# Optimization experiments

Hardware: AMD Instinct MI355X
Metric: run time of the kernel (lower is better)

The kernel has to match this reference:

```python
import jax, jax.numpy as jnp
import numpy as np

N, C, CI, H, W = 4, 512, 256, 64, 64  # batch, in_channels, inter_channels, spatial
EPS = 1e-5


def conv1x1(x, w, b):
    # x: (N,C,H,W), w: (O,C), b: (O,)
    return jnp.einsum('nchw,oc->nohw', x, w) + b[None, :, None, None]


def setup_inputs() -> dict:
    key = jax.random.key(0)
    ks = jax.random.split(key, 11)
    s = 0.02
    return {
        'x': jax.random.normal(ks[0], (N, C, H, W), dtype=jnp.float32),
        'g_w': jax.random.normal(ks[1], (CI, C), dtype=jnp.float32) * s,
        'g_b': jax.random.normal(ks[2], (CI,), dtype=jnp.float32) * s,
        'theta_w': jax.random.normal(ks[3], (CI, C), dtype=jnp.float32) * s,
        'theta_b': jax.random.normal(ks[4], (CI,), dtype=jnp.float32) * s,
        'phi_w': jax.random.normal(ks[5], (CI, C), dtype=jnp.float32) * s,
        'phi_b': jax.random.normal(ks[6], (CI,), dtype=jnp.float32) * s,
        'wz_w': jax.random.normal(ks[7], (C, CI), dtype=jnp.float32) * s,
        'wz_b': jax.random.normal(ks[8], (C,), dtype=jnp.float32) * s,
        'bn_gamma': jax.random.normal(ks[9], (C,), dtype=jnp.float32) * 0.1 + 1.0,
        'bn_beta': jax.random.normal(ks[10], (C,), dtype=jnp.float32) * 0.1,
    }


def reference(x, g_w, g_b, theta_w, theta_b, phi_w, phi_b, wz_w, wz_b, bn_gamma, bn_beta):
    # NLBlockND.forward_self, mode='embedded', dimension=2, bn_layer=True
    n = x.shape[0]
    L = x.shape[2] * x.shape[3]  # H*W tokens
    g_x = conv1x1(x, g_w, g_b).reshape(n, CI, L)          # (N,Ci,L)
    theta_x = conv1x1(x, theta_w, theta_b).reshape(n, CI, L)
    phi_x = conv1x1(x, phi_w, phi_b).reshape(n, CI, L)
    f = jnp.einsum('ncl,ncm->nlm', theta_x, phi_x)        # (N,L,L) = theta^T @ phi
    f_div_C = jax.nn.softmax(f, axis=-1)
    y = jnp.einsum('nlm,ncm->ncl', f_div_C, g_x)          # (N,Ci,L) = (attn @ g)^T
    y = y.reshape(n, CI, x.shape[2], x.shape[3])
    w_y = conv1x1(y, wz_w, wz_b)                          # (N,C,H,W)
    # BatchNorm2d, training-mode batch statistics (biased variance)
    mean = jnp.mean(w_y, axis=(0, 2, 3), keepdims=True)
    var = jnp.var(w_y, axis=(0, 2, 3), keepdims=True)
    w_y = (w_y - mean) * jax.lax.rsqrt(var + EPS)
    w_y = w_y * bn_gamma[None, :, None, None] + bn_beta[None, :, None, None]
    return w_y + x
```

## Files before the change

### kernel.cpp

```cpp
#include <hip/hip_runtime.h>
#include <hip/hip_bf16.h>
#include <hip/hip_fp16.h>


#define NB    4
#define CDIM  512
#define CIDIM 256
#define LDIM  4096
#define BN_EPS 1e-5f
#define LOG2E 1.4426950408889634f

typedef unsigned short u16;
typedef __attribute__((ext_vector_type(8))) short short8;
typedef __attribute__((ext_vector_type(4))) float f32x4;
typedef __attribute__((ext_vector_type(16))) float f32x16;

#define WY_OFF    0
#define THPH_OFF  8388608
#define G_OFF     12582912
#define Y_OFF     14680064
#define WTS_OFF   16777216
#define BIAS2_OFF 17039360
#define ML_OFF    17039872
#define ST_OFF    17105408

__device__ __forceinline__ u16 f2b(float f) {
    union { float f; unsigned u; } v; v.f = f;
    return (u16)((v.u + 0x7FFFu + ((v.u >> 16) & 1u)) >> 16);
}

__device__ __forceinline__ float b2f(u16 x) {
    return __uint_as_float((unsigned)x << 16);
}

__device__ __forceinline__ unsigned pack2(float a, float b) {
    return (unsigned)f2b(a) | ((unsigned)f2b(b) << 16);
}

__device__ __forceinline__ float fast_exp2(float x) {
#if __has_builtin(__builtin_amdgcn_exp2f)
    return __builtin_amdgcn_exp2f(x);
#else
    float r; asm("v_exp_f32 %0, %1" : "=v"(r) : "v"(x)); return r;
#endif
}

__device__ __forceinline__ void gl_lds16(const u16* g, u16* l) {
    __builtin_amdgcn_global_load_lds(
        (const __attribute__((address_space(1))) void*)g,
        (__attribute__((address_space(3))) void*)l, 16, 0, 0);
}

__global__ void transpose_x(const float* __restrict__ x, u16* __restrict__ xt) {
    __shared__ float tile[32][33];
    int n = blockIdx.z;
    int l0 = blockIdx.x * 32, c0 = blockIdx.y * 32;
    const float* xn = x + (size_t)n * CDIM * LDIM;
    u16* xtn = xt + (size_t)n * LDIM * CDIM;
    int tx = threadIdx.x, ty = threadIdx.y;
#pragma unroll
    for (int k = 0; k < 4; k++)
        tile[ty + 8 * k][tx] = xn[(size_t)(c0 + ty + 8 * k) * LDIM + l0 + tx];
    __syncthreads();
#pragma unroll
    for (int k = 0; k < 4; k++)
        xtn[(size_t)(l0 + ty + 8 * k) * CDIM + c0 + tx] = f2b(tile[tx][ty + 8 * k]);
}

__global__ void cast_w(const float* __restrict__ gw, const float* __restrict__ tw,
                       const float* __restrict__ pw, const float* __restrict__ zw,
                       u16* __restrict__ out,
                       const float* __restrict__ tb, const float* __restrict__ pb,
                       float* __restrict__ bc) {
    int idx = blockIdx.x * 256 + threadIdx.x;
    if (idx < 4 * 131072) {
        int seg = idx >> 17, off = idx & 131071;
        const float* s = (seg == 0) ? gw : (seg == 1) ? tw : (seg == 2) ? pw : zw;
        float v = s[off];
        if (seg == 1) v *= LOG2E;
        out[idx] = f2b(v);
    } else {
        int i = idx - 4 * 131072;
        if (i < 256) bc[i] = tb[i] * LOG2E;
        else if (i < 512) bc[i] = pb[i - 256];
    }
}

template <int BIAS_MODE, bool OUT_BF16>
__global__ __launch_bounds__(256)
void gemm_nt(const u16* __restrict__ A, const u16* __restrict__ B,
             void* __restrict__ Dv, const float* __restrict__ bias,
             int K, int lda, int ldb, int ldd,
             long batchA, long batchB, long batchD) {
    __shared__ __align__(16) u16 As[2][128 * 32];
    __shared__ __align__(16) u16 Bs[2][128 * 32];
    int z = blockIdx.z;
    A += (size_t)z * batchA;
    B += (size_t)z * batchB;

    int tid = threadIdx.x, lane = tid & 63, wave = tid >> 6;
    int n0 = blockIdx.x * 128, m0 = blockIdx.y * 128;
    int wr = wave >> 1, wc = wave & 1;

    f32x4 acc[4][4];
#pragma unroll
    for (int i = 0; i < 4; i++)
#pragma unroll
        for (int j = 0; j < 4; j++) acc[i][j] = (f32x4){0.f, 0.f, 0.f, 0.f};

    int sr = wave * 16 + (lane >> 2);
    int ss = ((lane & 3) ^ ((lane >> 2) & 3)) * 8;
    const u16* Ag0 = A + (size_t)(m0 + sr) * lda + ss;
    const u16* Ag1 = A + (size_t)(m0 + 64 + sr) * lda + ss;
    const u16* Bg0 = B + (size_t)(n0 + sr) * ldb + ss;
    const u16* Bg1 = B + (size_t)(n0 + 64 + sr) * ldb + ss;
    int sdst = wave * 16 * 32;

    int koff = ((lane >> 4) ^ (lane & 3)) * 8;
    int ra = (wr * 64 + (lane & 15)) * 32 + koff;
    int rb = (wc * 64 + (lane & 15)) * 32 + koff;

#define GSTAGE(bi, k0_) do {                                                   \
    gl_lds16(Ag0 + (k0_), &As[bi][sdst]);                                      \
    gl_lds16(Ag1 + (k0_), &As[bi][sdst + 2048]);                               \
    gl_lds16(Bg0 + (k0_), &Bs[bi][sdst]);                                      \
    gl_lds16(Bg1 + (k0_), &Bs[bi][sdst + 2048]);                               \
} while (0)

    GSTAGE(0, 0);
    int cur = 0;

    for (int k0 = 0; k0 < K; k0 += 32) {
        __syncthreads();
        if (k0 + 32 < K) GSTAGE(cur ^ 1, k0 + 32);

        short8 af[4], bf[4];
#pragma unroll
        for (int mt = 0; mt < 4; mt++) af[mt] = *(const short8*)&As[cur][ra + mt * 512];
#pragma unroll
        for (int nt = 0; nt < 4; nt++) bf[nt] = *(const short8*)&Bs[cur][rb + nt * 512];
#pragma unroll
        for (int mt = 0; mt < 4; mt++)
#pragma unroll
            for (int nt = 0; nt < 4; nt++)
                acc[mt][nt] = __builtin_amdgcn_mfma_f32_16x16x32_bf16(
                    af[mt], bf[nt], acc[mt][nt], 0, 0, 0);
        cur ^= 1;
    }
#undef GSTAGE

#pragma unroll
    for (int mt = 0; mt < 4; mt++) {
        int mg = m0 + wr * 64 + mt * 16 + (lane >> 4) * 4;
#pragma unroll
        for (int nt = 0; nt < 4; nt++) {
            int ng = n0 + wc * 64 + nt * 16 + (lane & 15);
#pragma unroll
            for (int r = 0; r < 4; r++) {
                float v = acc[mt][nt][r];
                if (BIAS_MODE == 1) v += bias[mg + r];
                if (BIAS_MODE == 2) v += bias[ng];
                if (OUT_BF16) {
                    u16* D = (u16*)Dv + (size_t)z * batchD;
                    D[(size_t)(mg + r) * ldd + ng] = f2b(v);
                } else {
                    float* D = (float*)Dv + (size_t)z * batchD;
                    D[(size_t)(mg + r) * ldd + ng] = v;
                }
            }
        }
    }
}

__global__ __launch_bounds__(256, 2)
void flash_attn(const u16* __restrict__ THPH, const u16* __restrict__ G,
                u16* __restrict__ OPB, unsigned* __restrict__ ML4) {
    __shared__ __align__(16) u16 Ks[2][32 * 256];
    __shared__ __align__(16) u16 Vs[2][256 * 32];

    int b = blockIdx.x;
    int n = b & 3;
    int jh = (b >> 2) & 3;
    int qt = b >> 4;
    int q0 = qt * 128;

    const u16* TH = THPH + (size_t)n * LDIM * 512;
    const u16* PH = TH + 256;
    const u16* Gn = G + (size_t)n * LDIM * CIDIM;
    u16* OPh = OPB + ((size_t)jh * NB + n) * CIDIM * LDIM;
    unsigned* MLh = ML4 + ((size_t)jh * NB + n) * LDIM;

    int tid = threadIdx.x, lane = tid & 63, w = tid >> 6;
    int h = lane >> 5, lq = lane & 31, l7 = lane & 7;

    short8 qf[16];
    {
        const u16* qb = TH + (size_t)(q0 + w * 32 + lq) * 512 + h * 8;
#pragma unroll
        for (int c = 0; c < 16; c++) qf[c] = *(const short8*)(qb + c * 16);
    }

    f32x16 o[8];
#pragma unroll
    for (int i = 0; i < 8; i++)
#pragma unroll
        for (int e = 0; e < 16; e++) o[i][e] = 0.f;
    float m = -3e38f, lsum = 0.f;

    int krh = lane >> 5;
    int ksl = lane & 31;
    int vr = lane >> 2;
    int vsl = (lane & 3) ^ ((lane >> 3) & 3);

#define STAGE(bufi, jt_) do {                                                  \
    int j0_ = jh * 1024 + (jt_) * 32;                                          \
    _Pragma("unroll")                                                          \
    for (int i = 0; i < 4; i++) {                                              \
        int r = w * 8 + 2 * i + krh;                                           \
        int s = ksl ^ (r & 7);                                                 \
        gl_lds16(PH + (size_t)(j0_ + r) * 512 + s * 8,                         \
                 &Ks[bufi][(w * 8 + 2 * i) * 256]);                            \
    }                                                                          \
    _Pragma("unroll")                                                          \
    for (int i = 0; i < 4; i++) {                                              \
        int r = w * 64 + 16 * i + vr;                                          \
        gl_lds16(Gn + (size_t)r * LDIM + j0_ + vsl * 8,                        \
                 &Vs[bufi][(w * 64 + 16 * i) * 32]);                           \
    }                                                                          \
} while (0)

    STAGE(0, 0);
    int cur = 0;

#pragma unroll 1
    for (int jt = 0; jt < 32; jt++) {
        __syncthreads();
        if (jt + 1 < 32) STAGE(cur ^ 1, jt + 1);

        const u16* kb = Ks[cur];
        const u16* vb = Vs[cur];

        f32x16 svx, svy;
#pragma unroll
        for (int e = 0; e < 16; e++) { svx[e] = 0.f; svy[e] = 0.f; }
#pragma unroll
        for (int c = 0; c < 8; c++) {
            int slot = (c * 2 + h) ^ l7;
            short8 ka = *(const short8*)&kb[lq * 256 + slot * 8];
            svx = __builtin_amdgcn_mfma_f32_32x32x16_bf16(ka, qf[c], svx, 0, 0, 0);
        }
#pragma unroll
        for (int c = 8; c < 16; c++) {
            int slot = (c * 2 + h) ^ l7;
            short8 ka = *(const short8*)&kb[lq * 256 + slot * 8];
            svy = __builtin_amdgcn_mfma_f32_32x32x16_bf16(ka, qf[c], svy, 0, 0, 0);
        }
        f32x16 sv = svx + svy;

        float tm = sv[0];
#pragma unroll
        for (int r = 1; r < 16; r++) tm = fmaxf(tm, sv[r]);
        tm = fmaxf(tm, __shfl_xor(tm, 32, 64));

        if (!__all(tm <= m + 11.5f)) {
            float mnew = fmaxf(m, tm);
            float al = fast_exp2(m - mnew);
            m = mnew;
            lsum *= al;
#pragma unroll
            for (int i = 0; i < 8; i++)
#pragma unroll
                for (int e = 0; e < 16; e++) o[i][e] *= al;
        }

        float rs = 0.f;
#pragma unroll
        for (int r = 0; r < 16; r++) {
            float p = fast_exp2(sv[r] - m);
            sv[r] = p;
            rs += p;
        }
        lsum += rs + __shfl_xor(rs, 32, 64);

#pragma unroll
        for (int st = 0; st < 2; st++) {
            int r0 = 8 * st;
            float e0 = sv[r0 + 0], e1 = sv[r0 + 1];
            float e2 = sv[r0 + 2], e3 = sv[r0 + 3];
            float e4 = sv[r0 + 4], e5 = sv[r0 + 5];
            float e6 = sv[r0 + 6], e7 = sv[r0 + 7];
            unsigned own_a = h ? pack2(e4, e5) : pack2(e0, e1);
            unsigned own_b = h ? pack2(e6, e7) : pack2(e2, e3);
            unsigned snd_a = h ? pack2(e0, e1) : pack2(e4, e5);
            unsigned snd_b = h ? pack2(e2, e3) : pack2(e6, e7);
            unsigned rcv_a = __shfl_xor(snd_a, 32, 64);
            unsigned rcv_b = __shfl_xor(snd_b, 32, 64);
            union { unsigned u[4]; short8 v; } pf;
            pf.u[0] = h ? rcv_a : own_a;
            pf.u[1] = h ? rcv_b : own_b;
            pf.u[2] = h ? own_a : rcv_a;
            pf.u[3] = h ? own_b : rcv_b;
            int slot = (st * 2 + h) ^ ((lq >> 1) & 3);
            short8 va[8];
#pragma unroll
            for (int cit = 0; cit < 8; cit++)
                va[cit] = *(const short8*)&vb[(cit * 32 + lq) * 32 + slot * 8];
#pragma unroll
            for (int cit = 0; cit < 8; cit++)
                o[cit] = __builtin_amdgcn_mfma_f32_32x32x16_bf16(va[cit], pf.v, o[cit], 0, 0, 0);
        }
        cur ^= 1;
    }

    int q = q0 + w * 32 + lq;
    if (h == 0) {
        unsigned pm = (unsigned)__half_as_ushort(__float2half(m));
        unsigned pl = (unsigned)__half_as_ushort(__float2half(lsum));
        MLh[q] = pm | (pl << 16);
    }
#pragma unroll
    for (int cit = 0; cit < 8; cit++)
#pragma unroll
        for (int rr = 0; rr < 16; rr++) {
            int ci = cit * 32 + (rr & 3) + 8 * (rr >> 2) + 4 * h;
            OPh[(size_t)ci * LDIM + q] = f2b(o[cit][rr]);
        }
#undef STAGE
}

__global__ void merge_y(const u16* __restrict__ OPB, const unsigned* __restrict__ ML4,
                        u16* __restrict__ Y) {
    __shared__ u16 tile[32][33];
    int nn = blockIdx.z;
    int l0 = blockIdx.x * 32, ci0 = blockIdx.y * 32;
    int tx = threadIdx.x, ty = threadIdx.y;
    int l = l0 + tx;

    float mq[4], lq[4];
#pragma unroll
    for (int q = 0; q < 4; q++) {
        unsigned u = ML4[((size_t)q * NB + nn) * LDIM + l];
        mq[q] = __half2float(__ushort_as_half((unsigned short)(u & 0xffff)));
        lq[q] = __half2float(__ushort_as_half((unsigned short)(u >> 16)));
    }
    float M = fmaxf(fmaxf(mq[0], mq[1]), fmaxf(mq[2], mq[3]));
    float wq[4];
    float den = 0.f;
#pragma unroll
    for (int q = 0; q < 4; q++) {
        wq[q] = fast_exp2(mq[q] - M);
        den += lq[q] * wq[q];
    }
    float inv = 1.f / den;
#pragma unroll
    for (int q = 0; q < 4; q++) wq[q] *= inv;

#pragma unroll
    for (int k = 0; k < 4; k++) {
        int ci = ci0 + ty + 8 * k;
        float acc = 0.f;
#pragma unroll
        for (int q = 0; q < 4; q++)
            acc += b2f(OPB[((size_t)q * NB + nn) * CIDIM * LDIM + (size_t)ci * LDIM + l]) * wq[q];
        tile[ty + 8 * k][tx] = f2b(acc);
    }
    __syncthreads();
    u16* Yn = Y + (size_t)nn * LDIM * CIDIM;
#pragma unroll
    for (int k = 0; k < 4; k++)
        Yn[(size_t)(l0 + ty + 8 * k) * CIDIM + ci0 + tx] = tile[tx][ty + 8 * k];
}

__global__ void bn_stats_kernel(const float* __restrict__ WY, float* __restrict__ stats) {
    int o = blockIdx.x, tid = threadIdx.x, lane = tid & 63, wave = tid >> 6;
    float s = 0.f, s2 = 0.f;
    for (int n = 0; n < NB; n++) {
        const float4* p = (const float4*)(WY + (size_t)(n * CDIM + o) * LDIM);
        for (int i = tid; i < LDIM / 4; i += 256) {
            float4 v = p[i];
            s += v.x + v.y + v.z + v.w;
            s2 += v.x * v.x + v.y * v.y + v.z * v.z + v.w * v.w;
        }
    }
    for (int o2 = 32; o2 > 0; o2 >>= 1) {
        s += __shfl_xor(s, o2, 64);
        s2 += __shfl_xor(s2, o2, 64);
    }
    __shared__ float rs[4], rs2[4];
    if (lane == 0) { rs[wave] = s; rs2[wave] = s2; }
    __syncthreads();
    if (tid == 0) {
        float S = rs[0] + rs[1] + rs[2] + rs[3];
        float S2 = rs2[0] + rs2[1] + rs2[2] + rs2[3];
        const float cnt = (float)(NB * LDIM);
        float mean = S / cnt;
        float var = S2 / cnt - mean * mean;
        stats[o] = mean;
        stats[CDIM + o] = rsqrtf(var + BN_EPS);
    }
}

__global__ void bn_apply_kernel(const float* __restrict__ WY, const float* __restrict__ stats,
                                const float* __restrict__ x,
                                const float* __restrict__ gamma, const float* __restrict__ beta,
                                float* __restrict__ out) {
    int i4 = blockIdx.x * 256 + threadIdx.x;
    int o = (i4 >> 10) & (CDIM - 1);
    float m = stats[o], is = stats[CDIM + o];
    float ga = gamma[o], be = beta[o];
    float4 w = ((const float4*)WY)[i4];
    float4 xv = ((const float4*)x)[i4];
    float4 r;
    r.x = (w.x - m) * is * ga + be + xv.x;
    r.y = (w.y - m) * is * ga + be + xv.y;
    r.z = (w.z - m) * is * ga + be + xv.z;
    r.w = (w.w - m) * is * ga + be + xv.w;
    ((float4*)out)[i4] = r;
}

extern "C" void kernel_launch(void* const* d_in, const int* in_sizes, int n_in,
                              void* d_out, int out_size, void* d_ws, size_t ws_size,
                              hipStream_t stream) {
    const float* x   = (const float*)d_in[0];
    const float* gw  = (const float*)d_in[1];
    const float* gb  = (const float*)d_in[2];
    const float* tw  = (const float*)d_in[3];
    const float* tb  = (const float*)d_in[4];
    const float* pw  = (const float*)d_in[5];
    const float* pb  = (const float*)d_in[6];
    const float* zw  = (const float*)d_in[7];
    const float* zb  = (const float*)d_in[8];
    const float* bng = (const float*)d_in[9];
    const float* bnb = (const float*)d_in[10];
    float* out = (float*)d_out;
    float* ws  = (float*)d_ws;

    float*    WY   = ws + WY_OFF;
    u16*      xT   = (u16*)(ws + WY_OFF);
    u16*      OPB  = (u16*)(ws + WY_OFF);
    u16*      THPH = (u16*)(ws + THPH_OFF);
    u16*      G    = (u16*)(ws + G_OFF);
    u16*      Y    = (u16*)(ws + Y_OFF);
    u16*      WB   = (u16*)(ws + WTS_OFF);
    float*    BC   = ws + BIAS2_OFF;
    unsigned* ML4  = (unsigned*)(ws + ML_OFF);
    float*    ST   = ws + ST_OFF;

    const long LC   = (long)LDIM * CDIM;
    const long LCI  = (long)LDIM * CIDIM;
    const long L512 = (long)LDIM * 512;
    const long CL   = (long)CDIM * LDIM;

    transpose_x<<<dim3(LDIM / 32, CDIM / 32, NB), dim3(32, 8), 0, stream>>>(x, xT);
    cast_w<<<2050, 256, 0, stream>>>(gw, tw, pw, zw, WB, tb, pb, BC);

    gemm_nt<2, true><<<dim3(4, 32, NB), 256, 0, stream>>>(
        xT, WB + 131072, THPH, BC, CDIM, CDIM, CDIM, 512, LC, 0, L512);
    gemm_nt<1, true><<<dim3(32, 2, NB), 256, 0, stream>>>(
        WB, xT, G, gb, CDIM, CDIM, CDIM, LDIM, 0, LC, LCI);

    flash_attn<<<dim3(512), 256, 0, stream>>>(THPH, G, OPB, ML4);
    merge_y<<<dim3(LDIM / 32, CIDIM / 32, NB), dim3(32, 8), 0, stream>>>(OPB, ML4, Y);

    gemm_nt<1, false><<<dim3(32, 4, NB), 256, 0, stream>>>(
        WB + 393216, Y, (void*)WY, zb, CIDIM, CIDIM, CIDIM, LDIM, 0, LCI, CL);

    bn_stats_kernel<<<dim3(CDIM), 256, 0, stream>>>(WY, ST);
    bn_apply_kernel<<<dim3(NB * CDIM * LDIM / 4 / 256), 256, 0, stream>>>(
        WY, ST, x, bng, bnb, out);
}
```

Baseline: 300.1 us.

## Fuse BatchNorm statistics into output GEMM epilogue and simplify attention MFMA chains

Per-channel sum and sum-of-squares are now accumulated in the epilogue of the final W_z GEMM. Each block reduces them with lane shuffles and shared-memory atomics, then adds them into global stats with atomics, and a tiny finalize kernel computes mean and rstd. This removes the separate bn_stats pass, which re-read the full 32 MB fp32 WY tensor. The flash-attention QK loop now uses a single MFMA accumulator chain instead of two, and V fragments are loaded inside the PV loop, which lowers register pressure but gives up some ILP. The global float atomics make the reduction order nondeterministic, and E[x^2]-mean^2 carries some precision risk.

Measured after the change: 275.7 us. -8.1%, faster.

```diff
diff --git a/kernel.cpp b/kernel.cpp
--- a/kernel.cpp
+++ b/kernel.cpp
@@ -71,7 +71,7 @@
                        const float* __restrict__ pw, const float* __restrict__ zw,
                        u16* __restrict__ out,
                        const float* __restrict__ tb, const float* __restrict__ pb,
-                       float* __restrict__ bc) {
+                       float* __restrict__ bc, float* __restrict__ st) {
     int idx = blockIdx.x * 256 + threadIdx.x;
     if (idx < 4 * 131072) {
         int seg = idx >> 17, off = idx & 131071;
@@ -83,17 +83,20 @@
         int i = idx - 4 * 131072;
         if (i < 256) bc[i] = tb[i] * LOG2E;
         else if (i < 512) bc[i] = pb[i - 256];
-    }
-}
-
-template <int BIAS_MODE, bool OUT_BF16>
+        else if (i < 1536) st[i - 512] = 0.f;
+    }
+}
+
+template <int BIAS_MODE, bool OUT_BF16, bool FUSE_STATS>
 __global__ __launch_bounds__(256)
 void gemm_nt(const u16* __restrict__ A, const u16* __restrict__ B,
              void* __restrict__ Dv, const float* __restrict__ bias,
+             float* __restrict__ stats,
              int K, int lda, int ldb, int ldd,
              long batchA, long batchB, long batchD) {
     __shared__ __align__(16) u16 As[2][128 * 32];
     __shared__ __align__(16) u16 Bs[2][128 * 32];
+    __shared__ float sred[256];
     int z = blockIdx.z;
     A += (size_t)z * batchA;
     B += (size_t)z * batchB;
@@ -149,9 +152,15 @@
     }
 #undef GSTAGE
 
+    if (FUSE_STATS) {
+        sred[tid] = 0.f;
+        __syncthreads();
+    }
+
 #pragma unroll
     for (int mt = 0; mt < 4; mt++) {
         int mg = m0 + wr * 64 + mt * 16 + (lane >> 4) * 4;
+        float ls[4] = {0.f, 0.f, 0.f, 0.f}, ls2[4] = {0.f, 0.f, 0.f, 0.f};
 #pragma unroll
         for (int nt = 0; nt < 4; nt++) {
             int ng = n0 + wc * 64 + nt * 16 + (lane & 15);
@@ -167,9 +176,44 @@
                     float* D = (float*)Dv + (size_t)z * batchD;
                     D[(size_t)(mg + r) * ldd + ng] = v;
                 }
+                if (FUSE_STATS) { ls[r] += v; ls2[r] += v * v; }
             }
         }
-    }
+        if (FUSE_STATS) {
+#pragma unroll
+            for (int r = 0; r < 4; r++) {
+                float s = ls[r], s2 = ls2[r];
+#pragma unroll
+                for (int msk = 1; msk <= 8; msk <<= 1) {
+                    s += __shfl_xor(s, msk, 64);
+                    s2 += __shfl_xor(s2, msk, 64);
+                }
+                if ((lane & 15) == 0) {
+                    int ch = wr * 64 + mt * 16 + (lane >> 4) * 4 + r;
+                    atomicAdd(&sred[ch], s);
+                    atomicAdd(&sred[128 + ch], s2);
+                }
+            }
+        }
+    }
+
+    if (FUSE_STATS) {
+        __syncthreads();
+        if (tid < 128) {
+            atomicAdd(&stats[m0 + tid], sred[tid]);
+            atomicAdd(&stats[CDIM + m0 + tid], sred[128 + tid]);
+        }
+    }
+}
+
+__global__ void bn_finalize(float* __restrict__ stats) {
+    int o = blockIdx.x * 256 + threadIdx.x;
+    if (o >= CDIM) return;
+    const float cnt = (float)(NB * LDIM);
+    float mean = stats[o] / cnt;
+    float var = stats[CDIM + o] / cnt - mean * mean;
+    stats[o] = mean;
+    stats[CDIM + o] = rsqrtf(var + BN_EPS);
 }
 
 __global__ __launch_bounds__(256, 2)
@@ -240,22 +284,15 @@
         const u16* kb = Ks[cur];
         const u16* vb = Vs[cur];
 
-        f32x16 svx, svy;
-#pragma unroll
-        for (int e = 0; e < 16; e++) { svx[e] = 0.f; svy[e] = 0.f; }
-#pragma unroll
-        for (int c = 0; c < 8; c++) {
+        f32x16 sv;
+#pragma unroll
+        for (int e = 0; e < 16; e++) sv[e] = 0.f;
+#pragma unroll
+        for (int c = 0; c < 16; c++) {
             int slot = (c * 2 + h) ^ l7;
             short8 ka = *(const short8*)&kb[lq * 256 + slot * 8];
-            svx = __builtin_amdgcn_mfma_f32_32x32x16_bf16(ka, qf[c], svx, 0, 0, 0);
-        }
-#pragma unroll
-        for (int c = 8; c < 16; c++) {
-            int slot = (c * 2 + h) ^ l7;
-            short8 ka = *(const short8*)&kb[lq * 256 + slot * 8];
-            svy = __builtin_amdgcn_mfma_f32_32x32x16_bf16(ka, qf[c], svy, 0, 0, 0);
-        }
-        f32x16 sv = svx + svy;
+            sv = __builtin_amdgcn_mfma_f32_32x32x16_bf16(ka, qf[c], sv, 0, 0, 0);
+        }
 
         float tm = sv[0];
 #pragma unroll
@@ -301,13 +338,11 @@
             pf.u[2] = h ? own_a : rcv_a;
             pf.u[3] = h ? own_b : rcv_b;
             int slot = (st * 2 + h) ^ ((lq >> 1) & 3);
-            short8 va[8];
-#pragma unroll
-            for (int cit = 0; cit < 8; cit++)
-                va[cit] = *(const short8*)&vb[(cit * 32 + lq) * 32 + slot * 8];
-#pragma unroll
-            for (int cit = 0; cit < 8; cit++)
-                o[cit] = __builtin_amdgcn_mfma_f32_32x32x16_bf16(va[cit], pf.v, o[cit], 0, 0, 0);
+#pragma unroll
+            for (int cit = 0; cit < 8; cit++) {
+                short8 va = *(const short8*)&vb[(cit * 32 + lq) * 32 + slot * 8];
+                o[cit] = __builtin_amdgcn_mfma_f32_32x32x16_bf16(va, pf.v, o[cit], 0, 0, 0);
+            }
         }
         cur ^= 1;
     }
@@ -369,35 +404,6 @@
 #pragma unroll
     for (int k = 0; k < 4; k++)
         Yn[(size_t)(l0 + ty + 8 * k) * CIDIM + ci0 + tx] = tile[tx][ty + 8 * k];
-}
-
-__global__ void bn_stats_kernel(const float* __restrict__ WY, float* __restrict__ stats) {
-    int o = blockIdx.x, tid = threadIdx.x, lane = tid & 63, wave = tid >> 6;
-    float s = 0.f, s2 = 0.f;
-    for (int n = 0; n < NB; n++) {
-        const float4* p = (const float4*)(WY + (size_t)(n * CDIM + o) * LDIM);
-        for (int i = tid; i < LDIM / 4; i += 256) {
-            float4 v = p[i];
-            s += v.x + v.y + v.z + v.w;
-            s2 += v.x * v.x + v.y * v.y + v.z * v.z + v.w * v.w;
-        }
-    }
-    for (int o2 = 32; o2 > 0; o2 >>= 1) {
-        s += __shfl_xor(s, o2, 64);
-        s2 += __shfl_xor(s2, o2, 64);
-    }
-    __shared__ float rs[4], rs2[4];
-    if (lane == 0) { rs[wave] = s; rs2[wave] = s2; }
-    __syncthreads();
-    if (tid == 0) {
-        float S = rs[0] + rs[1] + rs[2] + rs[3];
-        float S2 = rs2[0] + rs2[1] + rs2[2] + rs2[3];
-        const float cnt = (float)(NB * LDIM);
-        float mean = S / cnt;
-        float var = S2 / cnt - mean * mean;
-        stats[o] = mean;
-        stats[CDIM + o] = rsqrtf(var + BN_EPS);
-    }
 }
 
 __global__ void bn_apply_kernel(const float* __restrict__ WY, const float* __restrict__ stats,
@@ -452,20 +458,20 @@
     const long CL   = (long)CDIM * LDIM;
 
     transpose_x<<<dim3(LDIM / 32, CDIM / 32, NB), dim3(32, 8), 0, stream>>>(x, xT);
-    cast_w<<<2050, 256, 0, stream>>>(gw, tw, pw, zw, WB, tb, pb, BC);
-
-    gemm_nt<2, true><<<dim3(4, 32, NB), 256, 0, stream>>>(
-        xT, WB + 131072, THPH, BC, CDIM, CDIM, CDIM, 512, LC, 0, L512);
-    gemm_nt<1, true><<<dim3(32, 2, NB), 256, 0, stream>>>(
-        WB, xT, G, gb, CDIM, CDIM, CDIM, LDIM, 0, LC, LCI);
+    cast_w<<<2054, 256, 0, stream>>>(gw, tw, pw, zw, WB, tb, pb, BC, ST);
+
+    gemm_nt<2, true, false><<<dim3(4, 32, NB), 256, 0, stream>>>(
+        xT, WB + 131072, THPH, BC, nullptr, CDIM, CDIM, CDIM, 512, LC, 0, L512);
+    gemm_nt<1, true, false><<<dim3(32, 2, NB), 256, 0, stream>>>(
+        WB, xT, G, gb, nullptr, CDIM, CDIM, CDIM, LDIM, 0, LC, LCI);
 
     flash_attn<<<dim3(512), 256, 0, stream>>>(THPH, G, OPB, ML4);
     merge_y<<<dim3(LDIM / 32, CIDIM / 32, NB), dim3(32, 8), 0, stream>>>(OPB, ML4, Y);
 
-    gemm_nt<1, false><<<dim3(32, 4, NB), 256, 0, stream>>>(
-        WB + 393216, Y, (void*)WY, zb, CIDIM, CIDIM, CIDIM, LDIM, 0, LCI, CL);
-
-    bn_stats_kernel<<<dim3(CDIM), 256, 0, stream>>>(WY, ST);
+    gemm_nt<1, false, true><<<dim3(32, 4, NB), 256, 0, stream>>>(
+        WB + 393216, Y, (void*)WY, zb, ST, CIDIM, CIDIM, CIDIM, LDIM, 0, LCI, CL);
+
+    bn_finalize<<<2, 256, 0, stream>>>(ST);
     bn_apply_kernel<<<dim3(NB * CDIM * LDIM / 4 / 256), 256, 0, stream>>>(
         WY, ST, x, bng, bnb, out);
 }
```
